# Kernel optimization log

Hardware: AMD Instinct MI355X
Metric: run time of the kernel (lower is better)

Reference implementation:

```python
import jax, jax.numpy as jnp
import numpy as np

DIM = 1024
HEADS = 16
DH = 64          # dim_for_head
INNER = HEADS * DH
SCALE = DH ** -0.5


def setup_inputs() -> dict:
    key = jax.random.key(0)
    ks = jax.random.split(key, 5)
    x = jax.random.normal(ks[0], (4, 2048, DIM), dtype=jnp.float32)
    ln_gamma = jnp.ones((DIM,), dtype=jnp.float32)
    ln_beta = jnp.zeros((DIM,), dtype=jnp.float32)
    # torch Linear weight is [out, in]; store same layout, apply as x @ W.T
    w_qkv = jax.random.normal(ks[1], (3 * INNER, DIM), dtype=jnp.float32) * (DIM ** -0.5)
    w_out = jax.random.normal(ks[2], (DIM, INNER), dtype=jnp.float32) * (INNER ** -0.5)
    b_out = jnp.zeros((DIM,), dtype=jnp.float32)
    return {"x": x, "ln_gamma": ln_gamma, "ln_beta": ln_beta,
            "w_qkv": w_qkv, "w_out": w_out, "b_out": b_out}


def reference(x, ln_gamma, ln_beta, w_qkv, w_out, b_out):
    b, n, d = x.shape
    # LayerNorm (eps=1e-5 as torch default)
    mu = jnp.mean(x, axis=-1, keepdims=True)
    var = jnp.mean(jnp.square(x - mu), axis=-1, keepdims=True)
    xn = (x - mu) * jax.lax.rsqrt(var + 1e-5) * ln_gamma + ln_beta
    # QKV projection
    qkv = xn @ w_qkv.T                                   # [b, n, 3*inner]
    q, k, v = jnp.split(qkv, 3, axis=-1)
    reshape = lambda t: t.reshape(b, n, HEADS, DH).transpose(0, 2, 1, 3)  # [b, h, n, d]
    q, k, v = reshape(q), reshape(k), reshape(v)
    # Attention
    dots = jnp.einsum('bhqd,bhkd->bhqk', q, k) * SCALE
    attn = jax.nn.softmax(dots, axis=-1)                 # dropout p=0 -> identity
    out = jnp.einsum('bhqk,bhkd->bhqd', attn, v)
    out = out.transpose(0, 2, 1, 3).reshape(b, n, INNER)
    return out @ w_out.T + b_out
```

## Files before the change

kernel.cpp:

```cpp
#include <hip/hip_runtime.h>
#include <stdint.h>


typedef __attribute__((ext_vector_type(4)))  float  f32x4;
typedef __attribute__((ext_vector_type(16))) float  f32x16;
typedef __attribute__((ext_vector_type(8)))  short  s16x8;
typedef __attribute__((ext_vector_type(4)))  unsigned short u16x4;
typedef __attribute__((ext_vector_type(2)))  int    i32x2;
typedef __attribute__((ext_vector_type(4)))  int    i32x4;

__device__ __forceinline__ float bf2f(short b) {
    union { unsigned u; float f; } x; x.u = ((unsigned)(unsigned short)b) << 16; return x.f;
}
__device__ __forceinline__ short f2bf(float f) {
    union { float f; unsigned u; } x; x.f = f;
    unsigned r = x.u + 0x7fffu + ((x.u >> 16) & 1u);
    return (short)(r >> 16);
}
__device__ __forceinline__ float exp2_hw(float x) {
    float r; asm("v_exp_f32 %0, %1" : "=v"(r) : "v"(x)); return r;
}

__device__ __forceinline__ void gload_lds16(const void* g, void* l) {
    __builtin_amdgcn_global_load_lds(
        (const __attribute__((address_space(1))) void*)g,
        (__attribute__((address_space(3))) void*)l, 16, 0, 0);
}

__global__ void cvt_bf16(const float* __restrict__ in, short* __restrict__ out, int n4) {
    int i = blockIdx.x * blockDim.x + threadIdx.x;
    if (i >= n4) return;
    f32x4 v = ((const f32x4*)in)[i];
    u16x4 o;
    o.x = (unsigned short)f2bf(v.x); o.y = (unsigned short)f2bf(v.y);
    o.z = (unsigned short)f2bf(v.z); o.w = (unsigned short)f2bf(v.w);
    ((u16x4*)out)[i] = o;
}

__global__ void cvt_wqkv(const float* __restrict__ in, short* __restrict__ out, int n4) {
    int i = blockIdx.x * blockDim.x + threadIdx.x;
    if (i >= n4) return;
    const int row = i >> 8;
    const float sc = (row < 1024) ? 0.18033688011112042f : 1.0f;
    f32x4 v = ((const f32x4*)in)[i];
    u16x4 o;
    o.x = (unsigned short)f2bf(v.x * sc); o.y = (unsigned short)f2bf(v.y * sc);
    o.z = (unsigned short)f2bf(v.z * sc); o.w = (unsigned short)f2bf(v.w * sc);
    ((u16x4*)out)[i] = o;
}

__global__ __launch_bounds__(256)
void ln_kernel(const float* __restrict__ x, const float* __restrict__ gamma,
               const float* __restrict__ beta, short* __restrict__ xn) {
    const int w = threadIdx.x >> 6, l = threadIdx.x & 63;
    const size_t row = (size_t)blockIdx.x * 4 + w;
    const float* xr = x + row * 1024;
    f32x4 v[4];
    float sum = 0.f, ss = 0.f;
#pragma unroll
    for (int i = 0; i < 4; i++) {
        v[i] = *(const f32x4*)(xr + (l + 64 * i) * 4);
#pragma unroll
        for (int e = 0; e < 4; e++) { sum += v[i][e]; ss += v[i][e] * v[i][e]; }
    }
#pragma unroll
    for (int d = 1; d < 64; d <<= 1) { sum += __shfl_xor(sum, d); ss += __shfl_xor(ss, d); }
    const float mu   = sum * (1.f / 1024.f);
    const float var  = ss * (1.f / 1024.f) - mu * mu;
    const float rstd = rsqrtf(var + 1e-5f);
#pragma unroll
    for (int i = 0; i < 4; i++) {
        f32x4 g  = *(const f32x4*)(gamma + (l + 64 * i) * 4);
        f32x4 bt = *(const f32x4*)(beta  + (l + 64 * i) * 4);
        u16x4 o;
#pragma unroll
        for (int e = 0; e < 4; e++)
            o[e] = (unsigned short)f2bf((v[i][e] - mu) * rstd * g[e] + bt[e]);
        *(u16x4*)(xn + row * 1024 + (l + 64 * i) * 4) = o;
    }
}

template <int MODE, int NX>
__global__ __launch_bounds__(256)
void gemm_bt(const short* __restrict__ A, const short* __restrict__ W,
             short* __restrict__ outb, float* __restrict__ outf,
             const float* __restrict__ bias, int M, int N, int K) {
    __shared__ short Al[128 * 64];
    __shared__ short Bl[128 * 64];
    const int tid = threadIdx.x;
    const int w = tid >> 6, l = tid & 63;
    const int wr = w >> 1, wc = w & 1;
    const int nb = gridDim.x, bid = blockIdx.x;
    const int swz = (bid & 7) * (nb >> 3) + (bid >> 3);
    const int m0 = (swz / NX) * 128, n0 = (swz % NX) * 128;
    const int r8 = tid >> 3;
    const int c8 = tid & 7;

    f32x4 acc[4][4];
#pragma unroll
    for (int i = 0; i < 4; i++)
#pragma unroll
        for (int j = 0; j < 4; j++) acc[i][j] = (f32x4)0.f;

    for (int k0 = 0; k0 < K; k0 += 64) {
        __syncthreads();
#pragma unroll
        for (int p = 0; p < 4; p++) {
            const int row = p * 32 + r8;
            gload_lds16(A + (size_t)(m0 + row) * K + k0 + c8 * 8, Al + (p * 32 + w * 8) * 64);
            gload_lds16(W + (size_t)(n0 + row) * K + k0 + c8 * 8, Bl + (p * 32 + w * 8) * 64);
        }
        __syncthreads();
#pragma unroll
        for (int kc = 0; kc < 2; kc++) {
            const int ko = kc * 32 + (l >> 4) * 8;
            s16x8 af[4], bf[4];
#pragma unroll
            for (int i = 0; i < 4; i++)
                af[i] = *(const s16x8*)(Al + (wr * 64 + i * 16 + (l & 15)) * 64 + ko);
#pragma unroll
            for (int j = 0; j < 4; j++)
                bf[j] = *(const s16x8*)(Bl + (wc * 64 + j * 16 + (l & 15)) * 64 + ko);
#pragma unroll
            for (int i = 0; i < 4; i++)
#pragma unroll
                for (int j = 0; j < 4; j++)
                    acc[i][j] = __builtin_amdgcn_mfma_f32_16x16x32_bf16(af[i], bf[j], acc[i][j], 0, 0, 0);
        }
    }

    const int lr = (l >> 4) * 4, lc = l & 15;
#pragma unroll
    for (int j = 0; j < 4; j++) {
        const int cc = n0 + wc * 64 + j * 16 + lc;
        const float bv = (MODE == 1) ? bias[cc] : 0.f;
#pragma unroll
        for (int i = 0; i < 4; i++) {
            const int rb = m0 + wr * 64 + i * 16 + lr;
#pragma unroll
            for (int r = 0; r < 4; r++) {
                const float vv = acc[i][j][r];
                if (MODE == 0) outb[(size_t)(rb + r) * N + cc] = f2bf(vv);
                else           outf[(size_t)(rb + r) * N + cc] = vv + bv;
            }
        }
    }
}

__global__ __launch_bounds__(256)
void transpose_v(const short* __restrict__ qkv, short* __restrict__ vt) {
    __shared__ short T[64 * 72];
    const int tid = threadIdx.x;
    const int bh = blockIdx.y;
    const int b = bh >> 4, h = bh & 15;
    const int k0 = blockIdx.x * 64;
    const short* Vp = qkv + (size_t)b * 2048 * 3072 + 2048 + h * 64;
    const int r = tid >> 3, c = tid & 7;
#pragma unroll
    for (int p = 0; p < 2; p++) {
        const int k = p * 32 + r;
        s16x8 v = *(const s16x8*)(Vp + (size_t)(k0 + k) * 3072 + c * 8);
        *(s16x8*)(&T[k * 72 + c * 8]) = v;
    }
    __syncthreads();
#pragma unroll
    for (int p = 0; p < 2; p++) {
        const int d = p * 32 + r;
        s16x8 o;
#pragma unroll
        for (int e = 0; e < 8; e++) o[e] = T[(c * 8 + e) * 72 + d];
        *(s16x8*)(vt + ((size_t)bh * 64 + d) * 2048 + k0 + c * 8) = o;
    }
}

__global__ __launch_bounds__(256, 2)
void attn_kernel(const short* __restrict__ qkv, const short* __restrict__ vtg,
                 short* __restrict__ aout) {
    __shared__ short KV[2][2][64 * 64];
    const int tid = threadIdx.x, w = tid >> 6, l = tid & 63;
    const int bid = blockIdx.x;
    const int swz = (bid & 7) * 64 + (bid >> 3);
    const int qt = swz & 7, bh = swz >> 3;
    const int b = bh >> 4, h = bh & 15;
    const int q0 = qt * 256;
    const int y = l & 31, hi = l >> 5, l7 = l & 7;
    const short* Qp  = qkv + (size_t)b * 2048 * 3072 + h * 64;
    const short* Kp  = Qp + 1024;
    const short* Vtp = vtg + (size_t)bh * 64 * 2048;

    s16x8 bq[2][4];
#pragma unroll
    for (int u = 0; u < 2; u++) {
        const int qrow = q0 + w * 64 + u * 32 + y;
#pragma unroll
        for (int kc = 0; kc < 4; kc++)
            bq[u][kc] = *(const s16x8*)(Qp + (size_t)qrow * 3072 + kc * 16 + hi * 8);
    }

    f32x16 oc[2][2], ls[2];
#pragma unroll
    for (int u = 0; u < 2; u++) { oc[u][0] = (f32x16)0.f; oc[u][1] = (f32x16)0.f; ls[u] = (f32x16)0.f; }

    s16x8 ones;
#pragma unroll
    for (int e = 0; e < 8; e++) ones[e] = (short)0x3F80;

    const int srow = l >> 3;
    const int scs  = (l & 7) ^ srow;
    auto stage = [&](int par, int kv) {
#pragma unroll
        for (int p = 0; p < 2; p++) {
            const int row = w * 16 + p * 8 + srow;
            gload_lds16(Kp  + (size_t)(kv + row) * 3072 + scs * 8, &KV[par][0][(w * 16 + p * 8) * 64]);
            gload_lds16(Vtp + (size_t)row * 2048 + kv + scs * 8,   &KV[par][1][(w * 16 + p * 8) * 64]);
        }
    };

    const int Abase = y * 64 + ((hi ^ (l7 & 1)) * 8);
    int cofs[4];
#pragma unroll
    for (int j = 0; j < 4; j++) cofs[j] = ((l7 >> 1) ^ j) * 16;

    auto tilestep = [&](int par, int kv) {
        __syncthreads();
        if (kv + 64 < 2048) stage(par ^ 1, kv + 64);
        const short* Kb = &KV[par][0][0];
        const short* Vb = &KV[par][1][0];

        f32x16 s[2][2];
        s[0][0] = (f32x16)0.f; s[0][1] = (f32x16)0.f;
        s[1][0] = (f32x16)0.f; s[1][1] = (f32x16)0.f;
        __builtin_amdgcn_s_setprio(1);
#pragma unroll
        for (int kc = 0; kc < 4; kc++) {
#pragma unroll
            for (int kb = 0; kb < 2; kb++) {
                s16x8 ak = *(const s16x8*)(Kb + kb * 2048 + Abase + cofs[kc]);
                s[0][kb] = __builtin_amdgcn_mfma_f32_32x32x16_bf16(ak, bq[0][kc], s[0][kb], 0, 0, 0);
                s[1][kb] = __builtin_amdgcn_mfma_f32_32x32x16_bf16(ak, bq[1][kc], s[1][kb], 0, 0, 0);
            }
        }
        __builtin_amdgcn_s_setprio(0);

        int W0[2][2][8];
#pragma unroll
        for (int u = 0; u < 2; u++) {
#pragma unroll
            for (int kb = 0; kb < 2; kb++)
#pragma unroll
                for (int r = 0; r < 16; r++) s[u][kb][r] = exp2_hw(s[u][kb][r]);
#pragma unroll
            for (int kb = 0; kb < 2; kb++)
#pragma unroll
                for (int i = 0; i < 8; i++)
                    asm("v_cvt_pk_bf16_f32 %0, %1, %2"
                        : "=v"(W0[u][kb][i]) : "v"(s[u][kb][2 * i]), "v"(s[u][kb][2 * i + 1]));
        }

        __builtin_amdgcn_s_setprio(1);
#pragma unroll
        for (int a = 0; a < 2; a++)
#pragma unroll
            for (int bb = 0; bb < 2; bb++) {
                const int st = a * 2 + bb;
                s16x8 bv0 = *(const s16x8*)(Vb + 0 * 2048 + Abase + cofs[st]);
                s16x8 bv1 = *(const s16x8*)(Vb + 1 * 2048 + Abase + cofs[st]);
#pragma unroll
                for (int u = 0; u < 2; u++) {
                    i32x2 r0 = __builtin_amdgcn_permlane32_swap(W0[u][a][4 * bb + 0], W0[u][a][4 * bb + 2], false, false);
                    i32x2 r1 = __builtin_amdgcn_permlane32_swap(W0[u][a][4 * bb + 1], W0[u][a][4 * bb + 3], false, false);
                    union { i32x4 wv; s16x8 hv; } uu;
                    uu.wv = (i32x4){r0.x, r1.x, r0.y, r1.y};
                    ls[u]    = __builtin_amdgcn_mfma_f32_32x32x16_bf16(uu.hv, ones, ls[u], 0, 0, 0);
                    oc[u][0] = __builtin_amdgcn_mfma_f32_32x32x16_bf16(uu.hv, bv0, oc[u][0], 0, 0, 0);
                    oc[u][1] = __builtin_amdgcn_mfma_f32_32x32x16_bf16(uu.hv, bv1, oc[u][1], 0, 0, 0);
                }
            }
        __builtin_amdgcn_s_setprio(0);
    };

    stage(0, 0);
    for (int kv = 0; kv < 2048; kv += 128) {
        tilestep(0, kv);
        tilestep(1, kv + 64);
    }

#pragma unroll
    for (int u = 0; u < 2; u++)
#pragma unroll
        for (int r = 0; r < 16; r++) {
            const int qrr = (r & 3) + 8 * (r >> 2) + 4 * hi;
            const float ivr = 1.f / ls[u][r];
            const size_t row = (size_t)b * 2048 + q0 + w * 64 + u * 32 + qrr;
#pragma unroll
            for (int t2 = 0; t2 < 2; t2++)
                aout[row * 1024 + h * 64 + t2 * 32 + y] = f2bf(oc[u][t2][r] * ivr);
        }
}

extern "C" void kernel_launch(void* const* d_in, const int* in_sizes, int n_in,
                              void* d_out, int out_size, void* d_ws, size_t ws_size,
                              hipStream_t stream) {
    const float* x    = (const float*)d_in[0];
    const float* g    = (const float*)d_in[1];
    const float* be   = (const float*)d_in[2];
    const float* wqkv = (const float*)d_in[3];
    const float* wout = (const float*)d_in[4];
    const float* bo   = (const float*)d_in[5];
    float* out = (float*)d_out;

    char* ws = (char*)d_ws;
    short* xn    = (short*)(ws);
    short* wqkvb = (short*)(ws + 16777216);
    short* woutb = (short*)(ws + 16777216 + 6291456);
    short* qkvb  = (short*)(ws + 25165824);
    short* attb  = (short*)(ws + 75497472);
    short* vtg   = xn;

    cvt_wqkv<<<dim3(3072), 256, 0, stream>>>(wqkv, wqkvb, 3145728 / 4);
    cvt_bf16<<<dim3(1024), 256, 0, stream>>>(wout, woutb, 1048576 / 4);
    ln_kernel<<<dim3(2048), 256, 0, stream>>>(x, g, be, xn);
    gemm_bt<0, 24><<<dim3(1536), 256, 0, stream>>>(xn, wqkvb, qkvb, nullptr, nullptr, 8192, 3072, 1024);
    transpose_v<<<dim3(32, 64), 256, 0, stream>>>(qkvb, vtg);
    attn_kernel<<<dim3(512), 256, 0, stream>>>(qkvb, vtg, attb);
    gemm_bt<1, 8><<<dim3(512), 256, 0, stream>>>(attb, woutb, nullptr, out, bo, 8192, 1024, 1024);
}
```

Measured before the change: 206.4 us.

## Replace QKV projection GEMM with 256x192-tile double-buffered 512-thread kernel

Adds a new GEMM kernel for the QKV projection that uses 256x192 output tiles, 8 waves per block, double-buffered LDS staging via global_load_lds with XOR swizzle, and wave priority boosts around the MFMA bursts. The larger tiles raise arithmetic intensity per LDS load and cut global traffic compared to the old 128x128 kernel. The cost is heavy register use for 24 accumulators per lane, 112KB of dynamic shared memory per block, and extra barriers inside each k-step. The epilogue writes scalar bf16 stores, which may be uncoalesced.

```diff
diff --git a/kernel.cpp b/kernel.cpp
--- a/kernel.cpp
+++ b/kernel.cpp
@@ -77,6 +77,107 @@
         for (int e = 0; e < 4; e++)
             o[e] = (unsigned short)f2bf((v[i][e] - mu) * rstd * g[e] + bt[e]);
         *(u16x4*)(xn + row * 1024 + (l + 64 * i) * 4) = o;
+    }
+}
+
+template <int NX>
+__global__ __launch_bounds__(512, 2)
+void gemm256(const short* __restrict__ A, const short* __restrict__ W,
+             short* __restrict__ outb, int M, int N, int K) {
+    extern __shared__ short smem[];
+    short* Albuf = smem;
+    short* Blbuf = smem + 32768;
+    const int tid = threadIdx.x;
+    const int w = tid >> 6, l = tid & 63;
+    const int wr = w >> 2, wc = w & 3;
+    const int nb = gridDim.x, bid = blockIdx.x;
+    const int swz = (bid & 7) * (nb >> 3) + (bid >> 3);
+    const int m0 = (swz / NX) * 256, n0 = (swz % NX) * 192;
+    const int lx = l & 15, hi4 = l >> 4, l7 = l & 7;
+    const int srow = l >> 3;
+    const int scs  = (l & 7) ^ srow;
+
+    f32x4 acc[8][3];
+#pragma unroll
+    for (int i = 0; i < 8; i++)
+#pragma unroll
+        for (int j = 0; j < 3; j++) acc[i][j] = (f32x4)0.f;
+
+    auto STAGE = [&](int buf, int t) {
+        const int k0 = t * 64;
+#pragma unroll
+        for (int p = 0; p < 4; p++) {
+            const int row = p * 64 + w * 8 + srow;
+            gload_lds16(A + (size_t)(m0 + row) * K + k0 + scs * 8,
+                        Albuf + buf * 16384 + (p * 64 + w * 8) * 64);
+        }
+#pragma unroll
+        for (int p = 0; p < 3; p++) {
+            const int row = p * 64 + w * 8 + srow;
+            gload_lds16(W + (size_t)(n0 + row) * K + k0 + scs * 8,
+                        Blbuf + buf * 12288 + (p * 64 + w * 8) * 64);
+        }
+    };
+
+    STAGE(0, 0);
+    const int NT = K >> 6;
+    for (int t = 0; t < NT; ++t) {
+        const int cur = t & 1;
+        if (t + 1 < NT) {
+            STAGE(cur ^ 1, t + 1);
+            asm volatile("s_waitcnt vmcnt(7)" ::: "memory");
+        } else {
+            asm volatile("s_waitcnt vmcnt(0)" ::: "memory");
+        }
+        __builtin_amdgcn_s_barrier();
+        const short* Ab = Albuf + cur * 16384;
+        const short* Bb = Blbuf + cur * 12288;
+
+        s16x8 bfr[2][3];
+#pragma unroll
+        for (int kc = 0; kc < 2; kc++)
+#pragma unroll
+            for (int j = 0; j < 3; j++) {
+                const int R = wc * 48 + j * 16 + lx;
+                bfr[kc][j] = *(const s16x8*)(Bb + R * 64 + (((kc * 4 + hi4) ^ l7) * 8));
+            }
+
+#pragma unroll
+        for (int p = 0; p < 4; p++) {
+            s16x8 afr[2][2];
+#pragma unroll
+            for (int ii = 0; ii < 2; ii++)
+#pragma unroll
+                for (int kc = 0; kc < 2; kc++) {
+                    const int R = wr * 128 + (p * 2 + ii) * 16 + lx;
+                    afr[ii][kc] = *(const s16x8*)(Ab + R * 64 + (((kc * 4 + hi4) ^ l7) * 8));
+                }
+            __builtin_amdgcn_s_barrier();
+            __builtin_amdgcn_s_setprio(1);
+#pragma unroll
+            for (int kc = 0; kc < 2; kc++)
+#pragma unroll
+                for (int ii = 0; ii < 2; ii++)
+#pragma unroll
+                    for (int j = 0; j < 3; j++)
+                        acc[p * 2 + ii][j] = __builtin_amdgcn_mfma_f32_16x16x32_bf16(
+                            afr[ii][kc], bfr[kc][j], acc[p * 2 + ii][j], 0, 0, 0);
+            __builtin_amdgcn_s_setprio(0);
+            __builtin_amdgcn_s_barrier();
+        }
+    }
+
+    const int lr = hi4 * 4;
+#pragma unroll
+    for (int i = 0; i < 8; i++) {
+        const int rb = m0 + wr * 128 + i * 16 + lr;
+#pragma unroll
+        for (int j = 0; j < 3; j++) {
+            const int cc = n0 + wc * 48 + j * 16 + lx;
+#pragma unroll
+            for (int r = 0; r < 4; r++)
+                outb[(size_t)(rb + r) * N + cc] = f2bf(acc[i][j][r]);
+        }
     }
 }
 
@@ -317,10 +418,13 @@
     short* attb  = (short*)(ws + 75497472);
     short* vtg   = xn;
 
+    (void)hipFuncSetAttribute((const void*)gemm256<16>,
+                              hipFuncAttributeMaxDynamicSharedMemorySize, 114688);
+
     cvt_wqkv<<<dim3(3072), 256, 0, stream>>>(wqkv, wqkvb, 3145728 / 4);
     cvt_bf16<<<dim3(1024), 256, 0, stream>>>(wout, woutb, 1048576 / 4);
     ln_kernel<<<dim3(2048), 256, 0, stream>>>(x, g, be, xn);
-    gemm_bt<0, 24><<<dim3(1536), 256, 0, stream>>>(xn, wqkvb, qkvb, nullptr, nullptr, 8192, 3072, 1024);
+    gemm256<16><<<dim3(512), 512, 114688, stream>>>(xn, wqkvb, qkvb, 8192, 3072, 1024);
     transpose_v<<<dim3(32, 64), 256, 0, stream>>>(qkvb, vtg);
     attn_kernel<<<dim3(512), 256, 0, stream>>>(qkvb, vtg, attb);
     gemm_bt<1, 8><<<dim3(512), 256, 0, stream>>>(attb, woutb, nullptr, out, bo, 8192, 1024, 1024);
```

New measurement: 187.0 us. 1.1x faster.
